# Performance work log

Hardware: AMD Instinct MI355X
Metric: run time of the kernel (lower is better)

The kernel has to match this reference:

```python
import jax, jax.numpy as jnp
import numpy as np

B, N, L, Q = 10, 10, 256, 100
V, E, H = 365553, 200, 128


def _lstm_dir(x, Wi, Wh, b, rev):
    # x: [B,T,D] -> hidden states [B,T,H]; torch gate order i,f,g,o
    xg = jnp.einsum('btd,dk->btk', x, Wi) + b
    xg = jnp.swapaxes(xg, 0, 1)  # [T,B,4H]
    Bb = x.shape[0]
    Hh = Wh.shape[0]

    def step(carry, xt):
        h, c = carry
        g = xt + h @ Wh
        i, f, gg, o = jnp.split(g, 4, axis=-1)
        c = jax.nn.sigmoid(f) * c + jax.nn.sigmoid(i) * jnp.tanh(gg)
        h = jax.nn.sigmoid(o) * jnp.tanh(c)
        return (h, c), h

    init = (jnp.zeros((Bb, Hh), x.dtype), jnp.zeros((Bb, Hh), x.dtype))
    _, hs = jax.lax.scan(step, init, xg, reverse=rev)
    return jnp.swapaxes(hs, 0, 1)


def lstm_bi(x, Wi, Wh, b):
    return jnp.concatenate([_lstm_dir(x, Wi[0], Wh[0], b[0], False),
                            _lstm_dir(x, Wi[1], Wh[1], b[1], True)], axis=-1)


def setup_inputs():
    key = jax.random.key(0)
    ks = jax.random.split(key, 20)
    p = lambda k, s: jax.random.normal(k, s, jnp.float32) * 0.05
    return {
        'contents': jax.random.randint(ks[0], (B, N, L), 0, V),
        'question_ans': jax.random.randint(ks[1], (B, Q), 0, V),
        'logics': jnp.ones((B, 1), jnp.float32),
        'emb_fixed': p(ks[2], (V, E)),
        'emb_delta': p(ks[3], (V, E)),
        'ctx_Wi': p(ks[4], (2, E, 4 * H)), 'ctx_Wh': p(ks[5], (2, H, 4 * H)), 'ctx_b': p(ks[6], (2, 4 * H)),
        'qr_Wi': p(ks[7], (2, 2 * H + 2, 4 * H)), 'qr_Wh': p(ks[8], (2, H, 4 * H)), 'qr_b': p(ks[9], (2, 4 * H)),
        'cr_Wi': p(ks[10], (2, 4 * H + 2, 4 * H)), 'cr_Wh': p(ks[11], (2, H, 4 * H)), 'cr_b': p(ks[12], (2, 4 * H)),
        'gate_r_W': p(ks[13], (2 * H, 1)), 'gate_r_b': p(ks[14], (1,)),
        'gate_n_W': p(ks[15], (4 * H, 1)), 'gate_n_b': p(ks[16], (1,)),
        'dec_W': p(ks[17], (8 * H, 1)), 'dec_b': p(ks[18], (1,)),
    }


def _forward(contents, question_ans, logics, emb_fixed, emb_delta,
             ctx_Wi, ctx_Wh, ctx_b, qr_Wi, qr_Wh, qr_b, cr_Wi, cr_Wh, cr_b,
             gate_r_W, gate_r_b, gate_n_W, gate_n_b, dec_W, dec_b):
    # embeddings: fixed + trainable delta
    q_vec = emb_fixed[question_ans] + emb_delta[question_ans]            # [B,Q,200]
    q_enc = lstm_bi(q_vec, ctx_Wi, ctx_Wh, ctx_b)                        # [B,Q,256]
    c_tok = contents.reshape(B * N, L)
    c_vec = emb_fixed[c_tok] + emb_delta[c_tok]
    D_enc = lstm_bi(c_vec, ctx_Wi, ctx_Wh, ctx_b).reshape(B, N, L, 2 * H)  # [B,N,L,256]

    # reasoning gates (FC + sigmoid), +1e-8 as in source
    gate_q = jax.nn.sigmoid(q_enc @ gate_r_W + gate_r_b) + 1e-8          # [B,Q,1]
    gate_c = jax.nn.sigmoid(D_enc @ gate_r_W + gate_r_b) + 1e-8          # [B,N,L,1]

    # question-content matching matrix, all docs at once
    M_qc = jnp.einsum('bqd,bnld->bnql', q_enc, D_enc)                    # [B,N,Q,L]
    an = jax.nn.softmax(M_qc, axis=3)
    bn = jax.nn.softmax(M_qc, axis=2)
    RnQ = jnp.einsum('bnql,bnld->bnqd', an, D_enc)                       # [B,N,Q,256]
    RnD = jnp.einsum('bnql,bqd->bnld', bn, q_enc)                        # [B,N,L,256]
    D_RnD = jnp.concatenate([D_enc, RnD], axis=-1)                       # [B,N,L,512]
    feat_row = jnp.stack([M_qc.max(axis=2), M_qc.mean(axis=2)], axis=-1)  # [B,N,L,2]
    feat_col = jnp.stack([M_qc.max(axis=3), M_qc.mean(axis=3)], axis=-1)  # [B,N,Q,2]

    # cross-document attention: scores over all (position m, doc j) jointly per row
    Mx = jnp.einsum('bild,bjmd->bilmj', D_RnD, D_RnD)                    # [B,N,L,L,N]
    beta = jax.nn.softmax(Mx.reshape(B, N, L, L * N), axis=-1).reshape(B, N, L, L, N)
    RmD = jnp.einsum('bilmj,bjmd->bild', beta, D_RnD)                    # [B,N,L,512]

    RnQ_in = jnp.concatenate([RnQ, feat_col], axis=-1) * gate_q[:, None]  # [B,N,Q,258]
    RmD_in = jnp.concatenate([RmD, feat_row], axis=-1) * gate_c           # [B,N,L,514]

    q_out = lstm_bi(RnQ_in.reshape(B * N, Q, 2 * H + 2), qr_Wi, qr_Wh, qr_b).max(axis=1)
    c_out = lstm_bi(RmD_in.reshape(B * N, L, 4 * H + 2), cr_Wi, cr_Wh, cr_b).max(axis=1)
    feat = jnp.concatenate([q_out, c_out], axis=-1).reshape(B, N, 4 * H)  # [B,N,512]

    g = jax.nn.sigmoid(feat @ gate_n_W + gate_n_b)                        # [B,N,1]
    gf = feat * g
    dec_in = jnp.concatenate([gf.max(axis=1), gf.mean(axis=1)], axis=-1)  # [B,1024]
    dec = dec_in @ dec_W + dec_b                                          # [B,1]
    return (dec * logics).reshape(B // 5, 5)


def reference(contents, question_ans, logics, emb_fixed, emb_delta,
              ctx_Wi, ctx_Wh, ctx_b, qr_Wi, qr_Wh, qr_b, cr_Wi, cr_Wh, cr_b,
              gate_r_W, gate_r_b, gate_n_W, gate_n_b, dec_W, dec_b):
    return _forward(contents, question_ans, logics, emb_fixed, emb_delta,
                    ctx_Wi, ctx_Wh, ctx_b, qr_Wi, qr_Wh, qr_b, cr_Wi, cr_Wh, cr_b,
                    gate_r_W, gate_r_b, gate_n_W, gate_n_b, dec_W, dec_b)
```

## Files before the change

### kernel.cpp

```cpp
#include <hip/hip_runtime.h>
#include <cstdint>
#include <cstddef>

typedef __attribute__((ext_vector_type(8))) _Float16 half8;
typedef __attribute__((ext_vector_type(4))) float f32x4;

__device__ __forceinline__ float fexp(float x){ return __expf(x); }
__device__ __forceinline__ float sig_fast(float x){
  return __builtin_amdgcn_rcpf(1.f + __expf(-x));
}
__device__ __forceinline__ float tanh_fast(float x){
  return 2.f*__builtin_amdgcn_rcpf(1.f + __expf(-2.f*x)) - 1.f;
}
__device__ __forceinline__ float sigf(float x){ return 1.0f/(1.0f+expf(-x)); }

__device__ __forceinline__ void async_lds16(const _Float16* g, _Float16* l){
  __builtin_amdgcn_global_load_lds(
      (const __attribute__((address_space(1))) void*)g,
      (__attribute__((address_space(3))) void*)l, 16, 0, 0);
}

__global__ __launch_bounds__(64)
void k_sentinel(float* out, int n){ int i=threadIdx.x; if(i<n) out[i]=1.0e9f; }

__global__ __launch_bounds__(256)
void k_embed16u(const int* __restrict__ c_tok, const int* __restrict__ q_tok,
                const float* __restrict__ ef, const float* __restrict__ ed,
                _Float16* __restrict__ oh, _Float16* __restrict__ ol, int Kpad)
{
  int t = blockIdx.x; int e = threadIdx.x;
  if (e >= Kpad) return;
  _Float16 h = (_Float16)0.f, l = (_Float16)0.f;
  int tok = -1;
  if (t < 25600) tok = c_tok[t];
  else if (t < 26600) tok = q_tok[t - 25600];
  if (tok >= 0 && e < 200){
    long r = (long)tok*200 + e;
    float v = ef[r] + ed[r];
    h = (_Float16)v; l = (_Float16)(v - (float)h);
  }
  oh[(long)t*Kpad + e] = h;
  ol[(long)t*Kpad + e] = l;
}

__global__ __launch_bounds__(256)
void k_wsplit(const float* __restrict__ W, _Float16* __restrict__ th,
              _Float16* __restrict__ tl, int K, int Kpad)
{
  int n = blockIdx.x;
  int dir = n >> 9, col = n & 511;
  for (int k = threadIdx.x; k < Kpad; k += 256){
    _Float16 h = (_Float16)0.f, l = (_Float16)0.f;
    if (k < K){
      float v = W[((long)dir*K + k)*512 + col];
      h = (_Float16)v; l = (_Float16)(v - (float)h);
    }
    th[(long)n*Kpad + k] = h;
    tl[(long)n*Kpad + k] = l;
  }
}

#define MFMA16(a,b,c) __builtin_amdgcn_mfma_f32_16x16x32_f16(a,b,c,0,0,0)

__global__ __launch_bounds__(256, 2)
void k_mfma(const _Float16* __restrict__ Ahb, const _Float16* __restrict__ Alb,
            const _Float16* __restrict__ Bhb, const _Float16* __restrict__ Blb,
            float* __restrict__ Cb, int M, int K, int N, int ldc,
            long sA, long sB, long sC, int divA, int divB, int passes)
{
  const int z = blockIdx.z;
  const _Float16* Ah = Ahb + (long)(z/divA)*sA;
  const _Float16* Al = Alb + (long)(z/divA)*sA;
  const _Float16* Bh = Bhb + (long)(z/divB)*sB;
  const _Float16* Bl = Blb + (long)(z/divB)*sB;
  float* C = Cb + (long)z*sC;

  const int m0 = blockIdx.x*128, n0 = blockIdx.y*128;
  const int tid = threadIdx.x;
  const int lane = tid & 63, wave = tid >> 6;
  const int wm = wave >> 1, wn = wave & 1;

  __shared__ _Float16 lds[2][2048*8];

  f32x4 acc[4][4] = {};

  const int KT = K >> 5;
  const bool p3 = (passes == 3);

  auto STAGE = [&](int buf, int kt){
    const int k0 = kt*32;
    #pragma unroll
    for (int it = 0; it < 8; ++it){
      const int c  = it*256 + tid;
      const int op = it >> 1;
      const int kb = (c >> 7) & 3;
      const int row = c & 127;
      const _Float16* base = (op==0) ? Ah : (op==1) ? Al : (op==2) ? Bh : Bl;
      int gr = (op < 2) ? (m0 + row) : (n0 + row);
      if (op < 2 && gr >= M) gr = M - 1;
      const _Float16* src = base + (long)gr*K + k0 + kb*8;
      _Float16* dst = &lds[buf][(size_t)(it*256 + (tid & ~63))*8];
      async_lds16(src, dst);
    }
  };

  auto COMPUTE = [&](int buf){
    const int kb = lane >> 4, r = lane & 15;
    half8 ah[4], al[4], bh[4], bl[4];
    #pragma unroll
    for (int mi = 0; mi < 4; ++mi){
      ah[mi] = *(const half8*)&lds[buf][(size_t)(        kb*128 + wm*64 + mi*16 + r)*8];
      al[mi] = *(const half8*)&lds[buf][(size_t)( 512 + kb*128 + wm*64 + mi*16 + r)*8];
    }
    #pragma unroll
    for (int ni = 0; ni < 4; ++ni){
      bh[ni] = *(const half8*)&lds[buf][(size_t)(1024 + kb*128 + wn*64 + ni*16 + r)*8];
      bl[ni] = *(const half8*)&lds[buf][(size_t)(1536 + kb*128 + wn*64 + ni*16 + r)*8];
    }
    #pragma unroll
    for (int mi = 0; mi < 4; ++mi)
      #pragma unroll
      for (int ni = 0; ni < 4; ++ni){
        acc[mi][ni] = MFMA16(ah[mi], bh[ni], acc[mi][ni]);
        acc[mi][ni] = MFMA16(ah[mi], bl[ni], acc[mi][ni]);
        if (p3) acc[mi][ni] = MFMA16(al[mi], bh[ni], acc[mi][ni]);
      }
  };

  STAGE(0, 0);
  for (int kt = 0; kt < KT; ++kt){
    __syncthreads();
    if (kt + 1 < KT) STAGE((kt+1)&1, kt+1);
    COMPUTE(kt&1);
  }

  const int r4 = (lane >> 4) * 4, cN = lane & 15;
  #pragma unroll
  for (int mi = 0; mi < 4; ++mi)
    #pragma unroll
    for (int ni = 0; ni < 4; ++ni){
      const int row = m0 + wm*64 + mi*16 + r4;
      const int col = n0 + wn*64 + ni*16 + cN;
      #pragma unroll
      for (int r = 0; r < 4; ++r)
        if (row + r < M) C[(long)(row + r)*ldc + col] = acc[mi][ni][r];
    }
}

__global__ __launch_bounds__(512, 1)
void k_lstm2(const float* __restrict__ xg0, const float* __restrict__ Wh0,
             const float* __restrict__ bs0, float* __restrict__ out0,
             int S0, int T0, int ldx0,
             const float* __restrict__ xg1, const float* __restrict__ Wh1,
             const float* __restrict__ bs1, float* __restrict__ out1,
             int T1, int ldx1)
{
  const int bx = blockIdx.x;
  const int dir = blockIdx.y;
  const float* xg; const float* Whb; const float* bsb; float* out;
  int T, ldx, s;
  if (bx < S0){ s = bx;      xg = xg0; Whb = Wh0; bsb = bs0; out = out0; T = T0; ldx = ldx0; }
  else        { s = bx - S0; xg = xg1; Whb = Wh1; bsb = bs1; out = out1; T = T1; ldx = ldx1; }
  xg += dir*512;
  const float* Wh = Whb + (long)dir*128*512;
  const int dirOff = dir*128;
  const int k = threadIdx.x;
  const float bv = bsb[dir*512 + k];

  float4 wv[32];
  #pragma unroll
  for (int j = 0; j < 32; ++j){
    wv[j].x = Wh[(j*4+0)*512 + k];
    wv[j].y = Wh[(j*4+1)*512 + k];
    wv[j].z = Wh[(j*4+2)*512 + k];
    wv[j].w = Wh[(j*4+3)*512 + k];
  }

  __shared__ __align__(16) float h_lds[128];
  __shared__ float a_lds[512];
  float c = 0.f;
  if (k < 128) h_lds[k] = 0.f;
  __syncthreads();

  float gcur = xg[((long)s*T + (dir ? T-1 : 0))*ldx + k];

  for (int tt = 0; tt < T; ++tt) {
    const int t = dir ? (T-1-tt) : tt;
    float gnext = 0.f;
    if (tt + 1 < T){
      const int tn = dir ? (T-2-tt) : (tt+1);
      gnext = xg[((long)s*T + tn)*ldx + k];
    }
    float acc0 = gcur + bv, acc1 = 0.f, acc2 = 0.f, acc3 = 0.f;
    #pragma unroll
    for (int j = 0; j < 8; ++j) {
      float4 h0 = *(const float4*)&h_lds[(j*4+0)*4];
      float4 h1 = *(const float4*)&h_lds[(j*4+1)*4];
      float4 h2 = *(const float4*)&h_lds[(j*4+2)*4];
      float4 h3 = *(const float4*)&h_lds[(j*4+3)*4];
      acc0 += h0.x*wv[j*4+0].x + h0.y*wv[j*4+0].y + h0.z*wv[j*4+0].z + h0.w*wv[j*4+0].w;
      acc1 += h1.x*wv[j*4+1].x + h1.y*wv[j*4+1].y + h1.z*wv[j*4+1].z + h1.w*wv[j*4+1].w;
      acc2 += h2.x*wv[j*4+2].x + h2.y*wv[j*4+2].y + h2.z*wv[j*4+2].z + h2.w*wv[j*4+2].w;
      acc3 += h3.x*wv[j*4+3].x + h3.y*wv[j*4+3].y + h3.z*wv[j*4+3].z + h3.w*wv[j*4+3].w;
    }
    float g = (acc0 + acc1) + (acc2 + acc3);
    a_lds[k] = ((k >> 7) == 2) ? tanh_fast(g) : sig_fast(g);
    __syncthreads();
    if (k < 128) {
      float ig = a_lds[k];
      float fg = a_lds[k+128];
      float gg = a_lds[k+256];
      float og = a_lds[k+384];
      c = fg*c + ig*gg;
      float h = og*tanh_fast(c);
      h_lds[k] = h;
      out[((long)s*T + t)*256 + dirOff + k] = h;
    }
    __syncthreads();
    gcur = gnext;
  }
}

__global__ __launch_bounds__(256)
void k_gate(const float* __restrict__ in, const float* __restrict__ w,
            const float* __restrict__ b, float* __restrict__ out, int R)
{
  int row = blockIdx.x*4 + (threadIdx.x >> 6);
  int lane = threadIdx.x & 63;
  if (row >= R) return;
  const float* p = in + (long)row*256;
  float s = 0.f;
  #pragma unroll
  for (int j = 0; j < 4; ++j) s += p[lane + j*64]*w[lane + j*64];
  #pragma unroll
  for (int off = 32; off; off >>= 1) s += __shfl_down(s, off);
  if (lane == 0) out[row] = sigf(s + b[0]) + 1e-8f;
}

__global__ __launch_bounds__(256)
void k_an_feat16(const float* __restrict__ Mq, _Float16* __restrict__ anh,
                 _Float16* __restrict__ anl, float* __restrict__ feat)
{
  long r = blockIdx.x;
  int t = threadIdx.x;
  const int wid = t >> 6, lane = t & 63;
  float v = Mq[r*256 + t];
  float mx = v, sv = v;
  #pragma unroll
  for (int off = 32; off; off >>= 1){
    mx = fmaxf(mx, __shfl_down(mx, off));
    sv += __shfl_down(sv, off);
  }
  __shared__ float wmx[4], wsv[4], wse[4];
  if (lane == 0){ wmx[wid] = mx; wsv[wid] = sv; }
  __syncthreads();
  mx = fmaxf(fmaxf(wmx[0],wmx[1]), fmaxf(wmx[2],wmx[3]));
  sv = (wsv[0]+wsv[1]) + (wsv[2]+wsv[3]);
  float e = fexp(v - mx);
  float se = e;
  #pragma unroll
  for (int off = 32; off; off >>= 1) se += __shfl_down(se, off);
  if (lane == 0) wse[wid] = se;
  __syncthreads();
  se = (wse[0]+wse[1]) + (wse[2]+wse[3]);
  float a = e / se;
  _Float16 h = (_Float16)a;
  anh[r*256 + t] = h;
  anl[r*256 + t] = (_Float16)(a - (float)h);
  if (t == 0){ feat[r*2] = mx; feat[r*2+1] = sv*(1.f/256.f); }
}

__global__ __launch_bounds__(1024)
void k_bn_feat16(const float* __restrict__ Mq, _Float16* __restrict__ bth,
                 _Float16* __restrict__ btl, float* __restrict__ feat)
{
  int bn = blockIdx.x;
  int t = threadIdx.x;
  int l = t & 255, qg = t >> 8;
  const float* Mb = Mq + (long)bn*25600;
  const int q0 = qg*25, q1 = q0 + 25;
  float mx = -3.4e38f, sv = 0.f;
  for (int q = q0; q < q1; ++q){ float v = Mb[q*256 + l]; mx = fmaxf(mx, v); sv += v; }
  __shared__ float smx[4][256], ssv[4][256], sse[4][256];
  smx[qg][l] = mx; ssv[qg][l] = sv;
  __syncthreads();
  mx = fmaxf(fmaxf(smx[0][l],smx[1][l]), fmaxf(smx[2][l],smx[3][l]));
  sv = (ssv[0][l]+ssv[1][l]) + (ssv[2][l]+ssv[3][l]);
  float se = 0.f;
  for (int q = q0; q < q1; ++q) se += fexp(Mb[q*256 + l] - mx);
  sse[qg][l] = se;
  __syncthreads();
  se = (sse[0][l]+sse[1][l]) + (sse[2][l]+sse[3][l]);
  float inv = 1.f/se;
  long base = ((long)bn*256 + l)*128;
  for (int q = q0; q < q1; ++q){
    float a = fexp(Mb[q*256 + l] - mx)*inv;
    _Float16 h = (_Float16)a;
    bth[base + q] = h;
    btl[base + q] = (_Float16)(a - (float)h);
  }
  if (qg == 0){
    for (int q = 100; q < 128; ++q){ bth[base+q] = (_Float16)0.f; btl[base+q] = (_Float16)0.f; }
    long fr = (long)(bn*256 + l)*2;
    feat[fr] = mx; feat[fr+1] = sv*0.01f;
  }
}

__global__ __launch_bounds__(256)
void k_copy_to_x(const float* __restrict__ D, float* __restrict__ X)
{
  long idx = (long)blockIdx.x*256 + threadIdx.x;
  long r = idx >> 8; int d = idx & 255;
  X[r*512 + d] = D[idx];
}

__global__ __launch_bounds__(256)
void k_split_hl(const float* __restrict__ x, _Float16* __restrict__ h,
                _Float16* __restrict__ l, long n)
{
  long i = (long)blockIdx.x*256 + threadIdx.x;
  if (i >= n) return;
  float v = x[i];
  _Float16 hi = (_Float16)v;
  h[i] = hi;
  l[i] = (_Float16)(v - (float)hi);
}

__global__ __launch_bounds__(256)
void k_transp_hl(const float* __restrict__ src, _Float16* __restrict__ th,
                 _Float16* __restrict__ tl, int R, int Kp, long sSrc, long sDst)
{
  __shared__ float tile[32][33];
  const int m0 = blockIdx.x*32, n0 = blockIdx.y*32, z = blockIdx.z;
  const float* S = src + (long)z*sSrc;
  const int tx = threadIdx.x & 31, ty = threadIdx.x >> 5;
  #pragma unroll
  for (int r = 0; r < 32; r += 8){
    int gr = m0 + ty + r;
    tile[ty+r][tx] = (gr < R) ? S[(long)gr*256 + n0 + tx] : 0.f;
  }
  __syncthreads();
  const long base = (long)z*sDst;
  #pragma unroll
  for (int r = 0; r < 32; r += 8){
    float v = tile[tx][ty+r];
    _Float16 h = (_Float16)v;
    long o2 = base + (long)(n0+ty+r)*Kp + m0+tx;
    th[o2] = h;
    tl[o2] = (_Float16)(v - (float)h);
  }
}

__global__ __launch_bounds__(256)
void k_transpose_hl(const float* __restrict__ X, _Float16* __restrict__ Th,
                    _Float16* __restrict__ Tl)
{
  __shared__ float tile[32][33];
  const int m0 = blockIdx.x*32, n0 = blockIdx.y*32, b = blockIdx.z;
  const float* Xb = X + (long)b*2560*512;
  const int tx = threadIdx.x & 31, ty = threadIdx.x >> 5;
  #pragma unroll
  for (int r = 0; r < 32; r += 8)
    tile[ty+r][tx] = Xb[(long)(m0+ty+r)*512 + n0+tx];
  __syncthreads();
  const long base = (long)b*512*2560;
  #pragma unroll
  for (int r = 0; r < 32; r += 8){
    float v = tile[tx][ty+r];
    _Float16 h = (_Float16)v;
    long o2 = base + (long)(n0+ty+r)*2560 + m0+tx;
    Th[o2] = h;
    Tl[o2] = (_Float16)(v - (float)h);
  }
}

__global__ __launch_bounds__(256)
void k_softmax2560_hl2(const float* __restrict__ Sb, long sS,
                       _Float16* __restrict__ Shb, _Float16* __restrict__ Slb,
                       long sP)
{
  const int z = blockIdx.y;
  const float* p = Sb + z*sS + (long)blockIdx.x*2560;
  _Float16* Sh = Shb + z*sP;
  _Float16* Sl = Slb + z*sP;
  long r = blockIdx.x;
  int t = threadIdx.x;
  float loc[10];
  float mx = -3.4e38f;
  #pragma unroll
  for (int i=0;i<10;++i){ loc[i] = p[t + i*256]; mx = fmaxf(mx, loc[i]); }
  __shared__ float red[256];
  red[t]=mx; __syncthreads();
  for (int s2=128;s2;s2>>=1){ if(t<s2) red[t]=fmaxf(red[t],red[t+s2]); __syncthreads(); }
  mx = red[0]; __syncthreads();
  float se=0.f;
  #pragma unroll
  for (int i=0;i<10;++i){ loc[i]=fexp(loc[i]-mx); se+=loc[i]; }
  red[t]=se; __syncthreads();
  for (int s2=128;s2;s2>>=1){ if(t<s2) red[t]+=red[t+s2]; __syncthreads(); }
  float inv = 1.f/red[0];
  #pragma unroll
  for (int i=0;i<10;++i){
    float v = loc[i]*inv;
    _Float16 h = (_Float16)v;
    Sh[r*2560 + t + i*256] = h;
    Sl[r*2560 + t + i*256] = (_Float16)(v - (float)h);
  }
}

__global__ __launch_bounds__(320)
void k_build_rnq16(const float* __restrict__ RnQ, const float* __restrict__ featc,
                   const float* __restrict__ gq, _Float16* __restrict__ oh,
                   _Float16* __restrict__ ol)
{
  int row = blockIdx.x;
  int t = threadIdx.x;
  if (t >= 288) return;
  int b = row / 1000, q = row % 100;
  float g = gq[b*100 + q];
  float v = 0.f;
  if (t < 256)      v = RnQ[(long)row*256 + t]*g;
  else if (t < 258) v = featc[(long)row*2 + (t-256)]*g;
  _Float16 h = (_Float16)v;
  oh[(long)row*288 + t] = h;
  ol[(long)row*288 + t] = (_Float16)(v - (float)h);
}

__global__ __launch_bounds__(256)
void k_build_rmd16(const float* __restrict__ RmD, const float* __restrict__ featr,
                   const float* __restrict__ gc, _Float16* __restrict__ oh,
                   _Float16* __restrict__ ol)
{
  int row = blockIdx.x;
  float g = gc[row];
  for (int j = threadIdx.x; j < 544; j += 256){
    float v = 0.f;
    if (j < 512)      v = RmD[(long)row*512 + j]*g;
    else if (j < 514) v = featr[(long)row*2 + (j-512)]*g;
    _Float16 h = (_Float16)v;
    oh[(long)row*544 + j] = h;
    ol[(long)row*544 + j] = (_Float16)(v - (float)h);
  }
}

__global__ __launch_bounds__(256)
void k_maxt2(const float* __restrict__ hs0, float* __restrict__ o0, int S0, int T0,
             const float* __restrict__ hs1, float* __restrict__ o1, int T1)
{
  int x = blockIdx.x; int d = threadIdx.x;
  const float* hs; float* op; int T, s;
  if (x < S0){ hs = hs0; op = o0; T = T0; s = x; }
  else       { hs = hs1; op = o1; T = T1; s = x - S0; }
  float m = -3.4e38f;
  for (int t = 0; t < T; ++t) m = fmaxf(m, hs[((long)s*T + t)*256 + d]);
  op[s*256 + d] = m;
}

__global__ __launch_bounds__(512)
void k_final(const float* __restrict__ q_out, const float* __restrict__ c_out,
             const float* __restrict__ gnW, const float* __restrict__ gnB,
             const float* __restrict__ decW, const float* __restrict__ decB,
             const float* __restrict__ logics, float* __restrict__ out)
{
  int b = blockIdx.x;
  int t = threadIdx.x;
  __shared__ float red[512];
  float mx = -3.4e38f, sm = 0.f;
  for (int n = 0; n < 10; ++n) {
    int s = b*10 + n;
    float f = (t < 256) ? q_out[(long)s*256 + t] : c_out[(long)s*256 + (t-256)];
    red[t] = f * gnW[t]; __syncthreads();
    for (int st=256; st; st>>=1){ if (t<st) red[t]+=red[t+st]; __syncthreads(); }
    float g = sigf(red[0] + gnB[0]);
    __syncthreads();
    float gf = f*g;
    mx = fmaxf(mx, gf); sm += gf;
  }
  sm *= 0.1f;
  red[t] = mx*decW[t] + sm*decW[512 + t]; __syncthreads();
  for (int st=256; st; st>>=1){ if (t<st) red[t]+=red[t+st]; __syncthreads(); }
  if (t == 0) out[b] = (red[0] + decB[0]) * logics[b];
}

static inline int cdiv(int a, int b){ return (a + b - 1)/b; }

extern "C" void kernel_launch(void* const* d_in, const int* in_sizes, int n_in,
                              void* d_out, int out_size, void* d_ws, size_t ws_size,
                              hipStream_t stream)
{
  const int*   contents = (const int*)  d_in[0];
  const int*   qa       = (const int*)  d_in[1];
  const float* logics   = (const float*)d_in[2];
  const float* ef       = (const float*)d_in[3];
  const float* ed       = (const float*)d_in[4];
  const float* ctx_Wi   = (const float*)d_in[5];
  const float* ctx_Wh   = (const float*)d_in[6];
  const float* ctx_b    = (const float*)d_in[7];
  const float* qr_Wi    = (const float*)d_in[8];
  const float* qr_Wh    = (const float*)d_in[9];
  const float* qr_b     = (const float*)d_in[10];
  const float* cr_Wi    = (const float*)d_in[11];
  const float* cr_Wh    = (const float*)d_in[12];
  const float* cr_b     = (const float*)d_in[13];
  const float* grW      = (const float*)d_in[14];
  const float* grB      = (const float*)d_in[15];
  const float* gnW      = (const float*)d_in[16];
  const float* gnB      = (const float*)d_in[17];
  const float* decW     = (const float*)d_in[18];
  const float* decB     = (const float*)d_in[19];
  float* out = (float*)d_out;
  float* w = (float*)d_ws;

  const long RU = 26624;
  size_t o = 0;
  auto alloc = [&](size_t n){ size_t r = o; o += (n + 63) & ~(size_t)63; return r; };
  size_t cv16    = alloc((size_t)RU*224);
  size_t ctxW16  = alloc(1024u*224);
  size_t qrW16   = alloc(1024u*288);
  size_t crW16   = alloc(1024u*544);
  size_t c_xg    = alloc((size_t)RU*1024);
  size_t q_enc   = alloc(1000u*256);
  size_t D_enc   = alloc(25600u*256);
  size_t gate_q  = alloc(1000);
  size_t gate_c  = alloc(25600);
  size_t M_qc    = alloc(2560000);
  size_t an_     = alloc(2560000);
  size_t bn_     = alloc(3276800);
  size_t featc   = alloc(20000);
  size_t featr   = alloc(51200);
  size_t RnQ     = alloc(2560000);
  size_t Xb      = alloc(10u*2560*512);
  size_t Sbuf    = alloc(6553600);
  size_t RmD     = alloc(10u*2560*512);
  size_t rnq16   = alloc(10000u*288);
  size_t qr_xg   = alloc(10000u*1024);
  size_t q_hs    = alloc(100u*100*256);
  size_t rmd16   = alloc(25600u*544);
  size_t c_hs    = alloc(100u*256*256);
  size_t q_out   = alloc(100u*256);
  size_t c_out   = alloc(100u*256);

  if (ws_size < o*sizeof(float)) {
    k_sentinel<<<1,64,0,stream>>>(out, out_size);
    return;
  }

  _Float16* cvh = (_Float16*)(w + cv16);       _Float16* cvl = cvh + RU*224;
  _Float16* cWh = (_Float16*)(w + ctxW16);     _Float16* cWl = cWh + 1024L*224;
  _Float16* qWh = (_Float16*)(w + qrW16);      _Float16* qWl = qWh + 1024L*288;
  _Float16* rWh = (_Float16*)(w + crW16);      _Float16* rWl = rWh + 1024L*544;
  _Float16* nqh = (_Float16*)(w + rnq16);      _Float16* nql = nqh + 10000L*288;
  _Float16* mdh = (_Float16*)(w + rmd16);      _Float16* mdl = mdh + 25600L*544;
  _Float16* Xh  = (_Float16*)(w + c_xg);
  _Float16* Xl  = Xh  + 13107200L;
  _Float16* Xth = Xl  + 13107200L;
  _Float16* Xtl = Xth + 13107200L;
  _Float16* Sh  = (_Float16*)(w + M_qc);
  _Float16* Sl  = Sh + 6553600L;
  float*    S2  = w + qr_xg;
  _Float16* Sh2 = (_Float16*)(w + rmd16);
  _Float16* Sl2 = Sh2 + 6553600L;
  const long sS_pair = (long)(S2 - (w + Sbuf));
  const long sP_pair = (long)(Sh2 - Sh);
  _Float16* anh = (_Float16*)(w + an_);        _Float16* anl = anh + 2560000L;
  _Float16* bth = (_Float16*)(w + bn_);        _Float16* btl = bth + 3276800L;
  _Float16* D16h = (_Float16*)(w + RmD);       _Float16* D16l = D16h + 6553600L;
  _Float16* Dt16h = (_Float16*)(w + Sbuf);     _Float16* Dt16l = Dt16h + 6553600L;
  _Float16* q16h = (_Float16*)(w + q_hs);      _Float16* q16l = q16h + 256000L;
  _Float16* qt16h = q16l + 256000L;            _Float16* qt16l = qt16h + 327680L;
  float* q_xg_p = w + c_xg + 25600L*1024;

  k_wsplit<<<1024,256,0,stream>>>(ctx_Wi, cWh, cWl, 200, 224);
  k_wsplit<<<1024,256,0,stream>>>(qr_Wi,  qWh, qWl, 258, 288);
  k_wsplit<<<1024,256,0,stream>>>(cr_Wi,  rWh, rWl, 514, 544);
  k_embed16u<<<(int)RU, 256, 0, stream>>>(contents, qa, ef, ed, cvh, cvl, 224);

  k_mfma<<<dim3(208,8,1),256,0,stream>>>(cvh, cvl, cWh, cWl, w+c_xg,
      (int)RU, 224, 1024, 1024, 0L,0L,0L, 1,1, 3);

  k_lstm2<<<dim3(110,2),512,0,stream>>>(
      w+c_xg, ctx_Wh, ctx_b, w+D_enc, 100, 256, 1024,
      q_xg_p, ctx_Wh, ctx_b, w+q_enc, 100, 1024);

  k_gate<<<cdiv(1000,4),256,0,stream>>>(w+q_enc, grW, grB, w+gate_q, 1000);
  k_gate<<<cdiv(25600,4),256,0,stream>>>(w+D_enc, grW, grB, w+gate_c, 25600);

  k_split_hl<<<cdiv(6553600,256),256,0,stream>>>(w+D_enc, D16h, D16l, 6553600L);
  k_split_hl<<<cdiv(256000,256),256,0,stream>>>(w+q_enc, q16h, q16l, 256000L);
  k_transp_hl<<<dim3(8,8,100),256,0,stream>>>(w+D_enc, Dt16h, Dt16l, 256, 256, 65536L, 65536L);
  k_transp_hl<<<dim3(4,8,10),256,0,stream>>>(w+q_enc, qt16h, qt16l, 100, 128, 25600L, 32768L);

  k_mfma<<<dim3(1,2,100),256,0,stream>>>(q16h, q16l, D16h, D16l, w+M_qc,
      100, 256, 256, 256, 25600L, 65536L, 25600L, 10, 1, 3);

  k_an_feat16<<<10000,256,0,stream>>>(w+M_qc, anh, anl, w+featc);
  k_bn_feat16<<<100,1024,0,stream>>>(w+M_qc, bth, btl, w+featr);

  k_mfma<<<dim3(1,2,100),256,0,stream>>>(anh, anl, Dt16h, Dt16l, w+RnQ,
      100, 256, 256, 256, 25600L, 65536L, 25600L, 1, 1, 3);

  k_mfma<<<dim3(2,2,100),256,0,stream>>>(bth, btl, qt16h, qt16l, w+Xb+256,
      256, 128, 256, 512, 32768L, 32768L, 131072L, 1, 10, 3);

  k_copy_to_x<<<25600,256,0,stream>>>(w+D_enc, w+Xb);

  k_split_hl<<<51200,256,0,stream>>>(w+Xb, Xh, Xl, 13107200L);
  k_transpose_hl<<<dim3(80,16,10),256,0,stream>>>(w+Xb, Xth, Xtl);

  for (int bp = 0; bp < 5; ++bp) {
    const long xo = (long)bp*2*1310720;
    k_mfma<<<dim3(20,20,2),256,0,stream>>>(Xh+xo, Xl+xo, Xh+xo, Xl+xo, w+Sbuf,
        2560, 512, 2560, 2560, 1310720L, 1310720L, sS_pair, 1, 1, 2);
    k_softmax2560_hl2<<<dim3(2560,2),256,0,stream>>>(w+Sbuf, sS_pair, Sh, Sl, sP_pair);
    k_mfma<<<dim3(20,4,2),256,0,stream>>>(Sh, Sl, Xth+xo, Xtl+xo, w+RmD+xo,
        2560, 2560, 512, 512, sP_pair, 1310720L, 1310720L, 1, 1, 2);
  }

  k_build_rnq16<<<10000,320,0,stream>>>(w+RnQ, w+featc, w+gate_q, nqh, nql);
  k_mfma<<<dim3(79,8,1),256,0,stream>>>(nqh, nql, qWh, qWl, w+qr_xg,
      10000, 288, 1024, 1024, 0L,0L,0L, 1,1, 3);
  k_build_rmd16<<<25600,256,0,stream>>>(w+RmD, w+featr, w+gate_c, mdh, mdl);
  k_mfma<<<dim3(200,8,1),256,0,stream>>>(mdh, mdl, rWh, rWl, w+c_xg,
      25600, 544, 1024, 1024, 0L,0L,0L, 1,1, 3);

  k_lstm2<<<dim3(200,2),512,0,stream>>>(
      w+c_xg, cr_Wh, cr_b, w+c_hs, 100, 256, 1024,
      w+qr_xg, qr_Wh, qr_b, w+q_hs, 100, 1024);

  k_maxt2<<<200,256,0,stream>>>(w+c_hs, w+c_out, 100, 256, w+q_hs, w+q_out, 100);

  k_final<<<10,512,0,stream>>>(w+q_out, w+c_out, gnW, gnB, decW, decB, logics, out);
}
```

Baseline: 2.239 ms.

## Batch 16 sequences per LSTM block and use split-fp16 MFMA for recurrence

Replaces the per-sequence scalar LSTM recurrence kernel with one that processes 16 sequences per block. The recurrent h@Wh product runs on MFMA, using hi/lo fp16 splits of both h and a pre-split, transposed Wh held in registers, so three MFMAs approximate an fp32 product. This is meant to cut the per-step scalar FMA cost and the redundant per-sequence weight loads, and new k_wsplit launches prepare the recurrent weights. The trade-off is far fewer blocks (tens instead of hundreds), so most CUs sit idle on a latency-bound sequential loop, and each step carries more work per thread.

```diff
diff --git a/kernel.cpp b/kernel.cpp
--- a/kernel.cpp
+++ b/kernel.cpp
@@ -148,76 +148,112 @@
 }
 
 __global__ __launch_bounds__(512, 1)
-void k_lstm2(const float* __restrict__ xg0, const float* __restrict__ Wh0,
-             const float* __restrict__ bs0, float* __restrict__ out0,
-             int S0, int T0, int ldx0,
-             const float* __restrict__ xg1, const float* __restrict__ Wh1,
-             const float* __restrict__ bs1, float* __restrict__ out1,
-             int T1, int ldx1)
-{
-  const int bx = blockIdx.x;
-  const int dir = blockIdx.y;
-  const float* xg; const float* Whb; const float* bsb; float* out;
-  int T, ldx, s;
-  if (bx < S0){ s = bx;      xg = xg0; Whb = Wh0; bsb = bs0; out = out0; T = T0; ldx = ldx0; }
-  else        { s = bx - S0; xg = xg1; Whb = Wh1; bsb = bs1; out = out1; T = T1; ldx = ldx1; }
-  xg += dir*512;
-  const float* Wh = Whb + (long)dir*128*512;
+void k_lstm_mf(const float* __restrict__ xg0, const _Float16* __restrict__ W0h,
+               const _Float16* __restrict__ W0l, const float* __restrict__ bs0,
+               float* __restrict__ out0, int P0, int S0, int T0,
+               const float* __restrict__ xg1, const _Float16* __restrict__ W1h,
+               const _Float16* __restrict__ W1l, const float* __restrict__ bs1,
+               float* __restrict__ out1, int S1, int T1)
+{
+  const int bx = blockIdx.x, dir = blockIdx.y;
+  const float* xg; const _Float16 *Wth, *Wtl; const float* bsb; float* out;
+  int T, S, ch;
+  if (bx < P0){ ch = bx;      xg = xg0; Wth = W0h; Wtl = W0l; bsb = bs0; out = out0; T = T0; S = S0; }
+  else        { ch = bx - P0; xg = xg1; Wth = W1h; Wtl = W1l; bsb = bs1; out = out1; T = T1; S = S1; }
+  const int sbase = ch*16;
+  const int ns = (S - sbase < 16) ? (S - sbase) : 16;
+  const int tid = threadIdx.x, lane = tid & 63, wv = tid >> 6;
   const int dirOff = dir*128;
-  const int k = threadIdx.x;
-  const float bv = bsb[dir*512 + k];
-
-  float4 wv[32];
-  #pragma unroll
-  for (int j = 0; j < 32; ++j){
-    wv[j].x = Wh[(j*4+0)*512 + k];
-    wv[j].y = Wh[(j*4+1)*512 + k];
-    wv[j].z = Wh[(j*4+2)*512 + k];
-    wv[j].w = Wh[(j*4+3)*512 + k];
-  }
-
-  __shared__ __align__(16) float h_lds[128];
-  __shared__ float a_lds[512];
-  float c = 0.f;
-  if (k < 128) h_lds[k] = 0.f;
+
+  __shared__ _Float16 Ah[2048], Al[2048];
+  __shared__ float gat[16*512];
+
+  const _Float16* WH = Wth + (long)dir*512*128;
+  const _Float16* WL = Wtl + (long)dir*512*128;
+  half8 Bh[4][4], Bl[4][4];
+  #pragma unroll
+  for (int nt = 0; nt < 4; ++nt)
+    #pragma unroll
+    for (int kt = 0; kt < 4; ++kt){
+      long a = (long)(wv*64 + nt*16 + (lane & 15))*128 + kt*32 + (lane >> 4)*8;
+      Bh[nt][kt] = *(const half8*)&WH[a];
+      Bl[nt][kt] = *(const half8*)&WL[a];
+    }
+
+  const int k = tid & 127;
+  const int srow = tid >> 7;
+  float bv[4];
+  #pragma unroll
+  for (int g = 0; g < 4; ++g) bv[g] = bsb[dir*512 + g*128 + k];
+  float c[4] = {0.f, 0.f, 0.f, 0.f};
+  int sg[4];
+  #pragma unroll
+  for (int i = 0; i < 4; ++i){
+    int s = srow + 4*i;
+    sg[i] = sbase + (s < ns ? s : ns - 1);
+  }
+
+  for (int i = tid; i < 2048; i += 512){ Ah[i] = (_Float16)0.f; Al[i] = (_Float16)0.f; }
   __syncthreads();
 
-  float gcur = xg[((long)s*T + (dir ? T-1 : 0))*ldx + k];
-
-  for (int tt = 0; tt < T; ++tt) {
-    const int t = dir ? (T-1-tt) : tt;
-    float gnext = 0.f;
+  const int t0 = dir ? T-1 : 0;
+  float xc[4][4];
+  #pragma unroll
+  for (int i = 0; i < 4; ++i)
+    #pragma unroll
+    for (int g = 0; g < 4; ++g)
+      xc[i][g] = xg[((long)sg[i]*T + t0)*1024 + dir*512 + g*128 + k];
+
+  for (int tt = 0; tt < T; ++tt){
+    const int t = dir ? T-1-tt : tt;
+    float xn[4][4] = {};
     if (tt + 1 < T){
-      const int tn = dir ? (T-2-tt) : (tt+1);
-      gnext = xg[((long)s*T + tn)*ldx + k];
-    }
-    float acc0 = gcur + bv, acc1 = 0.f, acc2 = 0.f, acc3 = 0.f;
-    #pragma unroll
-    for (int j = 0; j < 8; ++j) {
-      float4 h0 = *(const float4*)&h_lds[(j*4+0)*4];
-      float4 h1 = *(const float4*)&h_lds[(j*4+1)*4];
-      float4 h2 = *(const float4*)&h_lds[(j*4+2)*4];
-      float4 h3 = *(const float4*)&h_lds[(j*4+3)*4];
-      acc0 += h0.x*wv[j*4+0].x + h0.y*wv[j*4+0].y + h0.z*wv[j*4+0].z + h0.w*wv[j*4+0].w;
-      acc1 += h1.x*wv[j*4+1].x + h1.y*wv[j*4+1].y + h1.z*wv[j*4+1].z + h1.w*wv[j*4+1].w;
-      acc2 += h2.x*wv[j*4+2].x + h2.y*wv[j*4+2].y + h2.z*wv[j*4+2].z + h2.w*wv[j*4+2].w;
-      acc3 += h3.x*wv[j*4+3].x + h3.y*wv[j*4+3].y + h3.z*wv[j*4+3].z + h3.w*wv[j*4+3].w;
-    }
-    float g = (acc0 + acc1) + (acc2 + acc3);
-    a_lds[k] = ((k >> 7) == 2) ? tanh_fast(g) : sig_fast(g);
+      const int tn = dir ? T-2-tt : tt+1;
+      #pragma unroll
+      for (int i = 0; i < 4; ++i)
+        #pragma unroll
+        for (int g = 0; g < 4; ++g)
+          xn[i][g] = xg[((long)sg[i]*T + tn)*1024 + dir*512 + g*128 + k];
+    }
+    f32x4 acc[4] = {};
+    #pragma unroll
+    for (int kt = 0; kt < 4; ++kt){
+      half8 a_h = *(const half8*)&Ah[((kt*4 + (lane >> 4))*16 + (lane & 15))*8];
+      half8 a_l = *(const half8*)&Al[((kt*4 + (lane >> 4))*16 + (lane & 15))*8];
+      #pragma unroll
+      for (int nt = 0; nt < 4; ++nt){
+        acc[nt] = MFMA16(a_h, Bh[nt][kt], acc[nt]);
+        acc[nt] = MFMA16(a_h, Bl[nt][kt], acc[nt]);
+        acc[nt] = MFMA16(a_l, Bh[nt][kt], acc[nt]);
+      }
+    }
+    #pragma unroll
+    for (int nt = 0; nt < 4; ++nt){
+      const int col = wv*64 + nt*16 + (lane & 15);
+      #pragma unroll
+      for (int r = 0; r < 4; ++r)
+        gat[((lane >> 4)*4 + r)*512 + col] = acc[nt][r];
+    }
     __syncthreads();
-    if (k < 128) {
-      float ig = a_lds[k];
-      float fg = a_lds[k+128];
-      float gg = a_lds[k+256];
-      float og = a_lds[k+384];
-      c = fg*c + ig*gg;
-      float h = og*tanh_fast(c);
-      h_lds[k] = h;
-      out[((long)s*T + t)*256 + dirOff + k] = h;
+    #pragma unroll
+    for (int i = 0; i < 4; ++i){
+      const int s = srow + 4*i;
+      float p0 = gat[s*512 +       k] + xc[i][0] + bv[0];
+      float p1 = gat[s*512 + 128 + k] + xc[i][1] + bv[1];
+      float p2 = gat[s*512 + 256 + k] + xc[i][2] + bv[2];
+      float p3 = gat[s*512 + 384 + k] + xc[i][3] + bv[3];
+      float ig = sig_fast(p0), fg = sig_fast(p1);
+      float gg = tanh_fast(p2), og = sig_fast(p3);
+      c[i] = fg*c[i] + ig*gg;
+      float h = og*tanh_fast(c[i]);
+      if (s < ns) out[((long)(sbase + s)*T + t)*256 + dirOff + k] = h;
+      _Float16 hh = (_Float16)h;
+      Ah[((k >> 3)*16 + s)*8 + (k & 7)] = hh;
+      Al[((k >> 3)*16 + s)*8 + (k & 7)] = (_Float16)(h - (float)hh);
+      xc[i][0] = xn[i][0]; xc[i][1] = xn[i][1];
+      xc[i][2] = xn[i][2]; xc[i][3] = xn[i][3];
     }
     __syncthreads();
-    gcur = gnext;
   }
 }
 
@@ -518,6 +554,9 @@
   size_t ctxW16  = alloc(1024u*224);
   size_t qrW16   = alloc(1024u*288);
   size_t crW16   = alloc(1024u*544);
+  size_t ctxWr   = alloc(131072);
+  size_t qrWr    = alloc(131072);
+  size_t crWr    = alloc(131072);
   size_t c_xg    = alloc((size_t)RU*1024);
   size_t q_enc   = alloc(1000u*256);
   size_t D_enc   = alloc(25600u*256);
@@ -549,6 +588,9 @@
   _Float16* cWh = (_Float16*)(w + ctxW16);     _Float16* cWl = cWh + 1024L*224;
   _Float16* qWh = (_Float16*)(w + qrW16);      _Float16* qWl = qWh + 1024L*288;
   _Float16* rWh = (_Float16*)(w + crW16);      _Float16* rWl = rWh + 1024L*544;
+  _Float16* cRh = (_Float16*)(w + ctxWr);      _Float16* cRl = cRh + 131072L;
+  _Float16* qRh = (_Float16*)(w + qrWr);       _Float16* qRl = qRh + 131072L;
+  _Float16* rRh = (_Float16*)(w + crWr);       _Float16* rRl = rRh + 131072L;
   _Float16* nqh = (_Float16*)(w + rnq16);      _Float16* nql = nqh + 10000L*288;
   _Float16* mdh = (_Float16*)(w + rmd16);      _Float16* mdl = mdh + 25600L*544;
   _Float16* Xh  = (_Float16*)(w + c_xg);
@@ -573,14 +615,17 @@
   k_wsplit<<<1024,256,0,stream>>>(ctx_Wi, cWh, cWl, 200, 224);
   k_wsplit<<<1024,256,0,stream>>>(qr_Wi,  qWh, qWl, 258, 288);
   k_wsplit<<<1024,256,0,stream>>>(cr_Wi,  rWh, rWl, 514, 544);
+  k_wsplit<<<1024,256,0,stream>>>(ctx_Wh, cRh, cRl, 128, 128);
+  k_wsplit<<<1024,256,0,stream>>>(qr_Wh,  qRh, qRl, 128, 128);
+  k_wsplit<<<1024,256,0,stream>>>(cr_Wh,  rRh, rRl, 128, 128);
   k_embed16u<<<(int)RU, 256, 0, stream>>>(contents, qa, ef, ed, cvh, cvl, 224);
 
   k_mfma<<<dim3(208,8,1),256,0,stream>>>(cvh, cvl, cWh, cWl, w+c_xg,
       (int)RU, 224, 1024, 1024, 0L,0L,0L, 1,1, 3);
 
-  k_lstm2<<<dim3(110,2),512,0,stream>>>(
-      w+c_xg, ctx_Wh, ctx_b, w+D_enc, 100, 256, 1024,
-      q_xg_p, ctx_Wh, ctx_b, w+q_enc, 100, 1024);
+  k_lstm_mf<<<dim3(8,2),512,0,stream>>>(
+      w+c_xg, cRh, cRl, ctx_b, w+D_enc, 7, 100, 256,
+      q_xg_p, cRh, cRl, ctx_b, w+q_enc, 10, 100);
 
   k_gate<<<cdiv(1000,4),256,0,stream>>>(w+q_enc, grW, grB, w+gate_q, 1000);
   k_gate<<<cdiv(25600,4),256,0,stream>>>(w+D_enc, grW, grB, w+gate_c, 25600);
@@ -623,9 +668,9 @@
   k_mfma<<<dim3(200,8,1),256,0,stream>>>(mdh, mdl, rWh, rWl, w+c_xg,
       25600, 544, 1024, 1024, 0L,0L,0L, 1,1, 3);
 
-  k_lstm2<<<dim3(200,2),512,0,stream>>>(
-      w+c_xg, cr_Wh, cr_b, w+c_hs, 100, 256, 1024,
-      w+qr_xg, qr_Wh, qr_b, w+q_hs, 100, 1024);
+  k_lstm_mf<<<dim3(14,2),512,0,stream>>>(
+      w+c_xg, rRh, rRl, cr_b, w+c_hs, 7, 100, 256,
+      w+qr_xg, qRh, qRl, qr_b, w+q_hs, 100, 100);
 
   k_maxt2<<<200,256,0,stream>>>(w+c_hs, w+c_out, 100, 256, w+q_hs, w+q_out, 100);
 
```

Measured after the change: 2.645 ms. 1.18x slower.

## Emit fp16 hi/lo scores from GEMM, batch attention five slabs per launch

Applied to the files above, without the earlier changes.

The score GEMM now writes hi/lo fp16 pairs straight from its epilogue, and the softmax reads and writes these fp16 pairs in place. This removes the fp32 score round trip. The attention loop now runs 2 iterations with 5 batch slabs per launch instead of 5 iterations of 2, giving larger grids and fewer launches. In 2-pass mode the GEMM also skips staging and reading the unused A-low operand. Splitting the scores before softmax loses a little precision compared with an fp32 input, and the larger per-launch scratch buffer relies on the workspace region at qr_xg being big enough.

```diff
diff --git a/kernel.cpp b/kernel.cpp
--- a/kernel.cpp
+++ b/kernel.cpp
@@ -66,14 +66,14 @@
 void k_mfma(const _Float16* __restrict__ Ahb, const _Float16* __restrict__ Alb,
             const _Float16* __restrict__ Bhb, const _Float16* __restrict__ Blb,
             float* __restrict__ Cb, int M, int K, int N, int ldc,
-            long sA, long sB, long sC, int divA, int divB, int passes)
+            long sA, long sB, long sC, int divA, int divB, int passes,
+            _Float16* __restrict__ Chb, _Float16* __restrict__ Clb, long sCh)
 {
   const int z = blockIdx.z;
   const _Float16* Ah = Ahb + (long)(z/divA)*sA;
   const _Float16* Al = Alb + (long)(z/divA)*sA;
   const _Float16* Bh = Bhb + (long)(z/divB)*sB;
   const _Float16* Bl = Blb + (long)(z/divB)*sB;
-  float* C = Cb + (long)z*sC;
 
   const int m0 = blockIdx.x*128, n0 = blockIdx.y*128;
   const int tid = threadIdx.x;
@@ -93,6 +93,7 @@
     for (int it = 0; it < 8; ++it){
       const int c  = it*256 + tid;
       const int op = it >> 1;
+      if (!p3 && op == 1) continue;
       const int kb = (c >> 7) & 3;
       const int row = c & 127;
       const _Float16* base = (op==0) ? Ah : (op==1) ? Al : (op==2) ? Bh : Bl;
@@ -110,7 +111,7 @@
     #pragma unroll
     for (int mi = 0; mi < 4; ++mi){
       ah[mi] = *(const half8*)&lds[buf][(size_t)(        kb*128 + wm*64 + mi*16 + r)*8];
-      al[mi] = *(const half8*)&lds[buf][(size_t)( 512 + kb*128 + wm*64 + mi*16 + r)*8];
+      if (p3) al[mi] = *(const half8*)&lds[buf][(size_t)( 512 + kb*128 + wm*64 + mi*16 + r)*8];
     }
     #pragma unroll
     for (int ni = 0; ni < 4; ++ni){
@@ -135,16 +136,38 @@
   }
 
   const int r4 = (lane >> 4) * 4, cN = lane & 15;
-  #pragma unroll
-  for (int mi = 0; mi < 4; ++mi)
+  if (Chb){
+    _Float16* Ch = Chb + (long)z*sCh;
+    _Float16* Cl = Clb + (long)z*sCh;
     #pragma unroll
-    for (int ni = 0; ni < 4; ++ni){
-      const int row = m0 + wm*64 + mi*16 + r4;
-      const int col = n0 + wn*64 + ni*16 + cN;
+    for (int mi = 0; mi < 4; ++mi)
       #pragma unroll
-      for (int r = 0; r < 4; ++r)
-        if (row + r < M) C[(long)(row + r)*ldc + col] = acc[mi][ni][r];
-    }
+      for (int ni = 0; ni < 4; ++ni){
+        const int row = m0 + wm*64 + mi*16 + r4;
+        const int col = n0 + wn*64 + ni*16 + cN;
+        #pragma unroll
+        for (int r = 0; r < 4; ++r)
+          if (row + r < M){
+            float v = acc[mi][ni][r];
+            _Float16 hh = (_Float16)v;
+            long idx = (long)(row + r)*ldc + col;
+            Ch[idx] = hh;
+            Cl[idx] = (_Float16)(v - (float)hh);
+          }
+      }
+  } else {
+    float* C = Cb + (long)z*sC;
+    #pragma unroll
+    for (int mi = 0; mi < 4; ++mi)
+      #pragma unroll
+      for (int ni = 0; ni < 4; ++ni){
+        const int row = m0 + wm*64 + mi*16 + r4;
+        const int col = n0 + wn*64 + ni*16 + cN;
+        #pragma unroll
+        for (int r = 0; r < 4; ++r)
+          if (row + r < M) C[(long)(row + r)*ldc + col] = acc[mi][ni][r];
+      }
+  }
 }
 
 __global__ __launch_bounds__(512, 1)
@@ -375,20 +398,22 @@
 }
 
 __global__ __launch_bounds__(256)
-void k_softmax2560_hl2(const float* __restrict__ Sb, long sS,
-                       _Float16* __restrict__ Shb, _Float16* __restrict__ Slb,
-                       long sP)
+void k_softmax2560_io16(_Float16* __restrict__ ShA, _Float16* __restrict__ SlA,
+                        long slab)
 {
   const int z = blockIdx.y;
-  const float* p = Sb + z*sS + (long)blockIdx.x*2560;
-  _Float16* Sh = Shb + z*sP;
-  _Float16* Sl = Slb + z*sP;
+  _Float16* Sh = ShA + (long)z*slab;
+  _Float16* Sl = SlA + (long)z*slab;
   long r = blockIdx.x;
   int t = threadIdx.x;
   float loc[10];
   float mx = -3.4e38f;
   #pragma unroll
-  for (int i=0;i<10;++i){ loc[i] = p[t + i*256]; mx = fmaxf(mx, loc[i]); }
+  for (int i=0;i<10;++i){
+    long idx = r*2560 + t + i*256;
+    loc[i] = (float)Sh[idx] + (float)Sl[idx];
+    mx = fmaxf(mx, loc[i]);
+  }
   __shared__ float red[256];
   red[t]=mx; __syncthreads();
   for (int s2=128;s2;s2>>=1){ if(t<s2) red[t]=fmaxf(red[t],red[t+s2]); __syncthreads(); }
@@ -403,8 +428,9 @@
   for (int i=0;i<10;++i){
     float v = loc[i]*inv;
     _Float16 h = (_Float16)v;
-    Sh[r*2560 + t + i*256] = h;
-    Sl[r*2560 + t + i*256] = (_Float16)(v - (float)h);
+    long idx = r*2560 + t + i*256;
+    Sh[idx] = h;
+    Sl[idx] = (_Float16)(v - (float)h);
   }
 }
 
@@ -555,13 +581,8 @@
   _Float16* Xl  = Xh  + 13107200L;
   _Float16* Xth = Xl  + 13107200L;
   _Float16* Xtl = Xth + 13107200L;
-  _Float16* Sh  = (_Float16*)(w + M_qc);
-  _Float16* Sl  = Sh + 6553600L;
-  float*    S2  = w + qr_xg;
-  _Float16* Sh2 = (_Float16*)(w + rmd16);
-  _Float16* Sl2 = Sh2 + 6553600L;
-  const long sS_pair = (long)(S2 - (w + Sbuf));
-  const long sP_pair = (long)(Sh2 - Sh);
+  _Float16* ShA = (_Float16*)(w + qr_xg);
+  _Float16* SlA = ShA + 5L*6553600L;
   _Float16* anh = (_Float16*)(w + an_);        _Float16* anl = anh + 2560000L;
   _Float16* bth = (_Float16*)(w + bn_);        _Float16* btl = bth + 3276800L;
   _Float16* D16h = (_Float16*)(w + RmD);       _Float16* D16l = D16h + 6553600L;
@@ -576,7 +597,7 @@
   k_embed16u<<<(int)RU, 256, 0, stream>>>(contents, qa, ef, ed, cvh, cvl, 224);
 
   k_mfma<<<dim3(208,8,1),256,0,stream>>>(cvh, cvl, cWh, cWl, w+c_xg,
-      (int)RU, 224, 1024, 1024, 0L,0L,0L, 1,1, 3);
+      (int)RU, 224, 1024, 1024, 0L,0L,0L, 1,1, 3, nullptr, nullptr, 0L);
 
   k_lstm2<<<dim3(110,2),512,0,stream>>>(
       w+c_xg, ctx_Wh, ctx_b, w+D_enc, 100, 256, 1024,
@@ -591,37 +612,38 @@
   k_transp_hl<<<dim3(4,8,10),256,0,stream>>>(w+q_enc, qt16h, qt16l, 100, 128, 25600L, 32768L);
 
   k_mfma<<<dim3(1,2,100),256,0,stream>>>(q16h, q16l, D16h, D16l, w+M_qc,
-      100, 256, 256, 256, 25600L, 65536L, 25600L, 10, 1, 3);
+      100, 256, 256, 256, 25600L, 65536L, 25600L, 10, 1, 3, nullptr, nullptr, 0L);
 
   k_an_feat16<<<10000,256,0,stream>>>(w+M_qc, anh, anl, w+featc);
   k_bn_feat16<<<100,1024,0,stream>>>(w+M_qc, bth, btl, w+featr);
 
   k_mfma<<<dim3(1,2,100),256,0,stream>>>(anh, anl, Dt16h, Dt16l, w+RnQ,
-      100, 256, 256, 256, 25600L, 65536L, 25600L, 1, 1, 3);
+      100, 256, 256, 256, 25600L, 65536L, 25600L, 1, 1, 3, nullptr, nullptr, 0L);
 
   k_mfma<<<dim3(2,2,100),256,0,stream>>>(bth, btl, qt16h, qt16l, w+Xb+256,
-      256, 128, 256, 512, 32768L, 32768L, 131072L, 1, 10, 3);
+      256, 128, 256, 512, 32768L, 32768L, 131072L, 1, 10, 3, nullptr, nullptr, 0L);
 
   k_copy_to_x<<<25600,256,0,stream>>>(w+D_enc, w+Xb);
 
   k_split_hl<<<51200,256,0,stream>>>(w+Xb, Xh, Xl, 13107200L);
   k_transpose_hl<<<dim3(80,16,10),256,0,stream>>>(w+Xb, Xth, Xtl);
 
-  for (int bp = 0; bp < 5; ++bp) {
-    const long xo = (long)bp*2*1310720;
-    k_mfma<<<dim3(20,20,2),256,0,stream>>>(Xh+xo, Xl+xo, Xh+xo, Xl+xo, w+Sbuf,
-        2560, 512, 2560, 2560, 1310720L, 1310720L, sS_pair, 1, 1, 2);
-    k_softmax2560_hl2<<<dim3(2560,2),256,0,stream>>>(w+Sbuf, sS_pair, Sh, Sl, sP_pair);
-    k_mfma<<<dim3(20,4,2),256,0,stream>>>(Sh, Sl, Xth+xo, Xtl+xo, w+RmD+xo,
-        2560, 2560, 512, 512, sP_pair, 1310720L, 1310720L, 1, 1, 2);
+  for (int half = 0; half < 2; ++half) {
+    const long xo = (long)half*5*1310720;
+    k_mfma<<<dim3(20,20,5),256,0,stream>>>(Xh+xo, Xl+xo, Xh+xo, Xl+xo, nullptr,
+        2560, 512, 2560, 2560, 1310720L, 1310720L, 0L, 1, 1, 2, ShA, SlA, 6553600L);
+    k_softmax2560_io16<<<dim3(2560,5),256,0,stream>>>(ShA, SlA, 6553600L);
+    k_mfma<<<dim3(20,4,5),256,0,stream>>>(ShA, SlA, Xth+xo, Xtl+xo, w+RmD+xo,
+        2560, 2560, 512, 512, 6553600L, 1310720L, 1310720L, 1, 1, 2,
+        nullptr, nullptr, 0L);
   }
 
   k_build_rnq16<<<10000,320,0,stream>>>(w+RnQ, w+featc, w+gate_q, nqh, nql);
   k_mfma<<<dim3(79,8,1),256,0,stream>>>(nqh, nql, qWh, qWl, w+qr_xg,
-      10000, 288, 1024, 1024, 0L,0L,0L, 1,1, 3);
+      10000, 288, 1024, 1024, 0L,0L,0L, 1,1, 3, nullptr, nullptr, 0L);
   k_build_rmd16<<<25600,256,0,stream>>>(w+RmD, w+featr, w+gate_c, mdh, mdl);
   k_mfma<<<dim3(200,8,1),256,0,stream>>>(mdh, mdl, rWh, rWl, w+c_xg,
-      25600, 544, 1024, 1024, 0L,0L,0L, 1,1, 3);
+      25600, 544, 1024, 1024, 0L,0L,0L, 1,1, 3, nullptr, nullptr, 0L);
 
   k_lstm2<<<dim3(200,2),512,0,stream>>>(
       w+c_xg, cr_Wh, cr_b, w+c_hs, 100, 256, 1024,
```

Result: faster. 1.874 ms (-16.3%).
